# Kernel optimization log

Hardware: AMD Instinct MI355X
Metric: run time of the kernel (lower is better)

## Reference

```python
import jax, jax.numpy as jnp
import numpy as np

BS, SL, CL = 32, 512, 20      # batch, seq_len (visits), codes per visit
D, H, V = 256, 4, 20000       # d_model, heads, vocab_size
HD = D // H                   # size_per_head = 64
EPS = 1e-5


def make_pe_table(d_model, max_pos):
    # torch PositionalEncoding: sinusoidal table with a zero pad row prepended
    pe = np.array([[pos / np.power(10000, 2.0 * (j // 2) / d_model)
                    for j in range(d_model)] for pos in range(max_pos)])
    pe[:, 0::2] = np.sin(pe[:, 0::2])
    pe[:, 1::2] = np.cos(pe[:, 1::2])
    pe = np.concatenate([np.zeros((1, d_model)), pe], axis=0)
    return jnp.asarray(pe, dtype=jnp.float32)  # [max_pos+1, d]


def layer_norm(x, g, b):
    mu = jnp.mean(x, axis=-1, keepdims=True)
    var = jnp.mean(jnp.square(x - mu), axis=-1, keepdims=True)
    return (x - mu) * jax.lax.rsqrt(var + EPS) * g + b


def setup_inputs() -> dict:
    key = jax.random.key(0)
    ks = jax.random.split(key, 12)
    input_seqs = jax.random.randint(ks[0], (BS, SL, CL), 0, V, dtype=jnp.int32)
    masks = jnp.ones((BS, SL, SL), dtype=jnp.int32)
    lengths = jax.random.randint(ks[1], (BS,), 1, SL + 1, dtype=jnp.int32)
    seq_time_step = jax.random.uniform(ks[2], (BS, SL), dtype=jnp.float32)
    code_masks = jax.random.uniform(ks[3], (BS, SL, CL), dtype=jnp.float32)

    emb_table = jax.random.normal(ks[4], (V + 1, D), dtype=jnp.float32) * 0.02
    emb_table = emb_table.at[V].set(0.0)  # padding_idx row (never indexed here)
    bound = 1.0 / np.sqrt(V)
    bias_emb = jax.random.uniform(ks[5], (D,), minval=-bound, maxval=bound, dtype=jnp.float32)
    s = 1.0 / np.sqrt(D)
    Wq = jax.random.uniform(ks[6], (D, D), minval=-s, maxval=s, dtype=jnp.float32)
    Wk = jax.random.uniform(ks[7], (D, D), minval=-s, maxval=s, dtype=jnp.float32)
    Wv = jax.random.uniform(ks[8], (D, D), minval=-s, maxval=s, dtype=jnp.float32)
    Wfc = jax.random.uniform(ks[9], (D, D), minval=-s, maxval=s, dtype=jnp.float32)
    ln_g = jnp.ones((D,), dtype=jnp.float32)
    ln_b = jnp.zeros((D,), dtype=jnp.float32)
    so = 1.0 / np.sqrt(4 * D)
    out_w = jax.random.uniform(ks[10], (2, 4 * D), minval=-so, maxval=so, dtype=jnp.float32)
    out_b = jax.random.uniform(ks[11], (2,), minval=-so, maxval=so, dtype=jnp.float32)
    pe_table = make_pe_table(D, SL)

    return dict(input_seqs=input_seqs, masks=masks, lengths=lengths,
                seq_time_step=seq_time_step, code_masks=code_masks,
                emb_table=emb_table, bias_emb=bias_emb, pe_table=pe_table,
                Wq=Wq, Wk=Wk, Wv=Wv, Wfc=Wfc, ln_g=ln_g, ln_b=ln_b,
                out_w=out_w, out_b=out_b)


def reference(input_seqs, masks, lengths, seq_time_step, code_masks,
              emb_table, bias_emb, pe_table, Wq, Wk, Wv, Wfc,
              ln_g, ln_b, out_w, out_b):
    bs, sl, _ = input_seqs.shape
    # visit embedding: sum of code embeddings + bias  -> [bs, sl, d]
    x = emb_table[input_seqs].sum(axis=2) + bias_emb
    # positional encoding: pos ids = 1..len, 0 beyond length
    t_idx = jnp.arange(sl, dtype=jnp.int32)
    pos_ids = jnp.where(t_idx[None, :] < lengths[:, None], t_idx[None, :] + 1, 0)
    x = x + pe_table[pos_ids]
    res = x
    # manual MHA -- NOTE faithful to original: view(bs, H, sl, hd) directly
    q = (x @ Wq.T).reshape(bs, H, sl, HD)
    k = (x @ Wk.T).reshape(bs, H, sl, HD)
    v = (x @ Wv.T).reshape(bs, H, sl, HD)
    energy = jnp.einsum('bhqd,bhkd->bhqk', q, k) / np.sqrt(HD)
    energy = jnp.where(masks[:, None, :, :] == 0, -jnp.inf, energy)
    attn = jax.nn.softmax(energy, axis=-1)
    o = jnp.einsum('bhqk,bhkd->bhqd', attn, v)          # [bs,H,sl,hd]
    o = o.transpose(0, 2, 1, 3).reshape(bs, sl, D)
    x = layer_norm(o @ Wfc.T + res, ln_g, ln_b)
    # zero out positions >= length
    valid = (t_idx[None, :] < lengths[:, None])          # [bs, sl]
    x = jnp.where(valid[:, :, None], x, 0.0)
    # triangular-weighted temporal pooling into 4 bins (vectorized loops)
    lens = lengths.astype(jnp.float32)
    t = jnp.arange(1, sl + 1, dtype=jnp.float32)
    s_val = 4.0 * t[None, :] / lens[:, None]             # [bs, sl]
    m = jnp.arange(1, 5, dtype=jnp.float32)              # 4 bins
    w = jnp.square(1.0 - jnp.abs(s_val[:, :, None] - m[None, None, :]) / 4.0)  # [bs,sl,4]
    U = jnp.einsum('bsm,bsd->bmd', w, x)                 # [bs,4,d]
    U = U.reshape(bs, 4 * D)
    return U @ out_w.T + out_b                           # [bs, 2]
```

## Files before the change

kernel.cpp:

```cpp
#include <hip/hip_runtime.h>

#define BSZ 32
#define SLEN 512
#define CLEN 20
#define DMOD 256
#define NH 4
#define HDIM 64

typedef _Float16 half8 __attribute__((ext_vector_type(8)));
typedef _Float16 half4 __attribute__((ext_vector_type(4)));
typedef float float4v __attribute__((ext_vector_type(4)));

#define MFMA16(a, b, c) __builtin_amdgcn_mfma_f32_16x16x32_f16(a, b, c, 0, 0, 0)
#define PG(fi) ((((fi) >> 4) * 17) + ((fi) & 15))

__global__ __launch_bounds__(256) void k_cast(
    const float* __restrict__ W0, const float* __restrict__ W1,
    const float* __restrict__ W2, const float* __restrict__ W3,
    const float* __restrict__ emb,
    _Float16* __restrict__ wh, _Float16* __restrict__ embh) {
  const int bid = blockIdx.x;
  const float* src;
  _Float16* dst;
  int idx;
  if (bid < 128) {
    const int z = bid >> 5;
    src = (z == 0) ? W0 : (z == 1) ? W1 : (z == 2) ? W2 : W3;
    dst = wh + (size_t)z * 65536;
    idx = ((bid & 31) * 256 + threadIdx.x) * 8;
  } else {
    src = emb;
    dst = embh;
    idx = ((bid - 128) * 256 + threadIdx.x) * 8;
  }
  float v[8];
  *(float4*)v = *(const float4*)(src + idx);
  *(float4*)(v + 4) = *(const float4*)(src + idx + 4);
  half8 h;
  #pragma unroll
  for (int i = 0; i < 8; ++i) h[i] = (_Float16)v[i];
  *(half8*)(dst + idx) = h;
}

__global__ __launch_bounds__(256) void k_embed(
    const int* __restrict__ seqs, const int* __restrict__ lengths,
    const _Float16* __restrict__ embh, const float* __restrict__ bias,
    const float* __restrict__ pe, _Float16* __restrict__ x) {
  const int row0 = blockIdx.x * 8;
  const int sub = threadIdx.x >> 5;
  const int hl = threadIdx.x & 31;
  const int row = row0 + sub;
  const int b = row >> 9, s = row & 511;
  __shared__ int codes[8][CLEN];
  if (threadIdx.x < 8 * CLEN)
    codes[threadIdx.x / CLEN][threadIdx.x % CLEN] = seqs[row0 * CLEN + threadIdx.x];
  __syncthreads();
  const int pos = (s < lengths[b]) ? (s + 1) : 0;
  const int d = hl * 8;
  float acc[8];
  *(float4*)acc = *(const float4*)(bias + d);
  *(float4*)(acc + 4) = *(const float4*)(bias + d + 4);
  const float4 pv0 = *(const float4*)(pe + (size_t)pos * DMOD + d);
  const float4 pv1 = *(const float4*)(pe + (size_t)pos * DMOD + d + 4);
  acc[0] += pv0.x; acc[1] += pv0.y; acc[2] += pv0.z; acc[3] += pv0.w;
  acc[4] += pv1.x; acc[5] += pv1.y; acc[6] += pv1.z; acc[7] += pv1.w;
  #pragma unroll
  for (int c = 0; c < CLEN; ++c) {
    const half8 ev = *(const half8*)(embh + (size_t)codes[sub][c] * DMOD + d);
    #pragma unroll
    for (int i = 0; i < 8; ++i) acc[i] += (float)ev[i];
  }
  half8 hv;
  #pragma unroll
  for (int i = 0; i < 8; ++i) hv[i] = (_Float16)acc[i];
  *(half8*)(x + (size_t)row * DMOD + d) = hv;
}

__global__ __launch_bounds__(256) void k_maskpack(
    const int* __restrict__ masks, unsigned int* __restrict__ pk) {
  const int row0 = blockIdx.x * 8;
  const int wv = threadIdx.x >> 6;
  const int lane = threadIdx.x & 63;
  #pragma unroll
  for (int p = 0; p < 16; ++p) {
    const int it = wv + p * 4;
    const int r = row0 + (it >> 3);
    const int chunk = it & 7;
    const int m = masks[(size_t)r * SLEN + chunk * 64 + lane];
    const unsigned long long bal = __ballot(m != 0);
    if (lane == 0) {
      pk[(size_t)r * 16 + chunk * 2]     = (unsigned int)bal;
      pk[(size_t)r * 16 + chunk * 2 + 1] = (unsigned int)(bal >> 32);
    }
  }
}

__global__ __launch_bounds__(256) void k_gemm_qkv(
    const _Float16* __restrict__ A, const _Float16* __restrict__ Wb,
    _Float16* __restrict__ q, _Float16* __restrict__ k, _Float16* __restrict__ v) {
  const int z = blockIdx.z;
  _Float16* Cb = (z == 0) ? q : (z == 1) ? k : v;
  const _Float16* w_ = Wb + (size_t)z * 65536;
  const int m0 = blockIdx.x * 128;
  const int n0 = blockIdx.y * 128;
  const int tid = threadIdx.x;
  const int lane = tid & 63;
  const int w = tid >> 6;
  const int wm = (w >> 1) * 4;
  const int wn = (w & 1) * 4;
  __shared__ _Float16 smem[8704];
  half8* As = (half8*)(smem);
  half8* Ws = (half8*)(smem + 4096);
  float4v acc[4][4];
  #pragma unroll
  for (int i = 0; i < 4; ++i)
    #pragma unroll
    for (int j = 0; j < 4; ++j)
      acc[i][j] = (float4v){0.f, 0.f, 0.f, 0.f};
  int li_[2]; size_t ga_[2], gw_[2];
  #pragma unroll
  for (int p = 0; p < 2; ++p) {
    const int c = tid + p * 256;
    const int r = c & 127, qd = c >> 7;
    li_[p] = (r >> 4) * 64 + qd * 16 + (r & 15);
    ga_[p] = (size_t)(m0 + r) * DMOD + qd * 8;
    gw_[p] = (size_t)(n0 + r) * DMOD + qd * 8;
  }
  half8 pa[2], pw[2];
  #pragma unroll
  for (int p = 0; p < 2; ++p) {
    pa[p] = *(const half8*)(A + ga_[p]);
    pw[p] = *(const half8*)(w_ + gw_[p]);
  }
  for (int k0 = 0; k0 < DMOD; k0 += 32) {
    #pragma unroll
    for (int p = 0; p < 2; ++p) {
      As[li_[p]] = pa[p];
      Ws[li_[p]] = pw[p];
    }
    __syncthreads();
    if (k0 + 32 < DMOD) {
      #pragma unroll
      for (int p = 0; p < 2; ++p) {
        pa[p] = *(const half8*)(A + ga_[p] + k0 + 32);
        pw[p] = *(const half8*)(w_ + gw_[p] + k0 + 32);
      }
    }
    half8 af[4], wf[4];
    #pragma unroll
    for (int i = 0; i < 4; ++i) {
      af[i] = As[(wm + i) * 64 + lane];
      wf[i] = Ws[(wn + i) * 64 + lane];
    }
    #pragma unroll
    for (int i = 0; i < 4; ++i)
      #pragma unroll
      for (int j = 0; j < 4; ++j)
        acc[i][j] = MFMA16(af[i], wf[j], acc[i][j]);
    __syncthreads();
  }
  const int cr = (lane >> 4) * 4;
  const int cc = lane & 15;
  _Float16* Eh = smem;
  #pragma unroll
  for (int ip = 0; ip < 4; ++ip) {
    #pragma unroll
    for (int j = 0; j < 4; ++j) {
      const int col = (wn + j) * 16 + cc;
      #pragma unroll
      for (int r = 0; r < 4; ++r)
        Eh[((w >> 1) * 16 + cr + r) * 136 + col] = (_Float16)acc[ip][j][r];
    }
    __syncthreads();
    #pragma unroll
    for (int e = 0; e < 2; ++e) {
      const int idx = tid + e * 256;
      const int lr = idx >> 4;
      const int cg = idx & 15;
      const int gr = m0 + (lr >> 4) * 64 + ip * 16 + (lr & 15);
      *(half8*)(Cb + (size_t)gr * DMOD + n0 + cg * 8) =
          *(const half8*)&Eh[lr * 136 + cg * 8];
    }
    __syncthreads();
  }
}

__global__ __launch_bounds__(256) void k_vt(
    const _Float16* __restrict__ v, _Float16* __restrict__ vt) {
  const int bh = blockIdx.x;
  const size_t off = (size_t)bh * 32768;
  __shared__ _Float16 Th[64][66];
  const int tid = threadIdx.x;
  const int sc = blockIdx.y * 64;
  #pragma unroll
  for (int p = 0; p < 2; ++p) {
    const int lin = tid + p * 256;
    const int r = lin >> 3, g = lin & 7;
    *(half8*)&Th[r][g * 8] = *(const half8*)(v + off + (size_t)(sc + r) * 64 + g * 8);
  }
  __syncthreads();
  #pragma unroll
  for (int p = 0; p < 2; ++p) {
    const int lin = tid + p * 256;
    const int d = lin >> 3, sg = lin & 7;
    half8 hv;
    #pragma unroll
    for (int j = 0; j < 8; ++j) hv[j] = Th[sg * 8 + j][d];
    *(half8*)(vt + off + (size_t)d * 512 + sc + sg * 8) = hv;
  }
}

__global__ __launch_bounds__(256) void k_gemm_fc(
    const _Float16* __restrict__ A, const _Float16* __restrict__ w_,
    float* __restrict__ C, const _Float16* __restrict__ res) {
  const int m0 = blockIdx.x * 128;
  const int n0 = blockIdx.y * 128;
  const int tid = threadIdx.x;
  const int lane = tid & 63;
  const int w = tid >> 6;
  const int wm = (w >> 1) * 4;
  const int wn = (w & 1) * 4;
  __shared__ half8 As[512], Ws[512];
  float4v acc[4][4];
  #pragma unroll
  for (int i = 0; i < 4; ++i)
    #pragma unroll
    for (int j = 0; j < 4; ++j)
      acc[i][j] = (float4v){0.f, 0.f, 0.f, 0.f};
  int li_[2]; size_t ga_[2], gw_[2];
  #pragma unroll
  for (int p = 0; p < 2; ++p) {
    const int c = tid + p * 256;
    const int r = c & 127, qd = c >> 7;
    li_[p] = (r >> 4) * 64 + qd * 16 + (r & 15);
    ga_[p] = (size_t)(m0 + r) * DMOD + qd * 8;
    gw_[p] = (size_t)(n0 + r) * DMOD + qd * 8;
  }
  half8 pa[2], pw[2];
  #pragma unroll
  for (int p = 0; p < 2; ++p) {
    pa[p] = *(const half8*)(A + ga_[p]);
    pw[p] = *(const half8*)(w_ + gw_[p]);
  }
  for (int k0 = 0; k0 < DMOD; k0 += 32) {
    #pragma unroll
    for (int p = 0; p < 2; ++p) {
      As[li_[p]] = pa[p];
      Ws[li_[p]] = pw[p];
    }
    __syncthreads();
    if (k0 + 32 < DMOD) {
      #pragma unroll
      for (int p = 0; p < 2; ++p) {
        pa[p] = *(const half8*)(A + ga_[p] + k0 + 32);
        pw[p] = *(const half8*)(w_ + gw_[p] + k0 + 32);
      }
    }
    half8 af[4], wf[4];
    #pragma unroll
    for (int i = 0; i < 4; ++i) {
      af[i] = As[(wm + i) * 64 + lane];
      wf[i] = Ws[(wn + i) * 64 + lane];
    }
    #pragma unroll
    for (int i = 0; i < 4; ++i)
      #pragma unroll
      for (int j = 0; j < 4; ++j)
        acc[i][j] = MFMA16(af[i], wf[j], acc[i][j]);
    __syncthreads();
  }
  const int cr = (lane >> 4) * 4;
  const int cc = lane & 15;
  #pragma unroll
  for (int i = 0; i < 4; ++i) {
    const int gm = m0 + (wm + i) * 16 + cr;
    #pragma unroll
    for (int j = 0; j < 4; ++j) {
      const int gc = n0 + (wn + j) * 16 + cc;
      #pragma unroll
      for (int r = 0; r < 4; ++r) {
        const size_t flat = (size_t)(gm + r) * DMOD + gc;
        C[flat] = acc[i][j][r] + (float)res[flat];
      }
    }
  }
}

__global__ __launch_bounds__(256, 2) void k_attn(
    const _Float16* __restrict__ q_, const _Float16* __restrict__ k_,
    const _Float16* __restrict__ vt, const unsigned int* __restrict__ pk,
    _Float16* __restrict__ o) {
  const int L = blockIdx.x;
  const int bh = (L & 7) * 16 + ((L >> 3) & 15);
  const int q0 = (L >> 7) * 128;
  const size_t bhoff = (size_t)bh * 32768;
  __shared__ half8 QP[1088];
  __shared__ half8 Ks[544], Vs[544];
  __shared__ unsigned long long Ms64[128];
  __shared__ float Ps[4][128];
  __shared__ float lsum[128];
  const int tid = threadIdx.x;
  const int w = tid >> 6;
  const int lane = tid & 63;
  const int l15 = lane & 15;
  const int quad = lane >> 4;
  #pragma unroll
  for (int p = 0; p < 4; ++p) {
    const int lin = tid + p * 256;
    const int r = lin >> 3, g = lin & 7;
    const int fi = (r >> 4) * 128 + g * 16 + (r & 15);
    QP[PG(fi)] = *(const half8*)(q_ + bhoff + (size_t)(q0 + r) * 64 + g * 8);
  }
  __syncthreads();
  half8 qf[8][2];
  #pragma unroll
  for (int ns = 0; ns < 8; ++ns) {
    const int gq = ns * 8 + quad;
    qf[ns][0] = QP[gq * 17 + l15];
    qf[ns][1] = QP[(gq + 4) * 17 + l15];
  }
  float4v oacc[8];
  float lsw[8] = {0.f, 0.f, 0.f, 0.f, 0.f, 0.f, 0.f, 0.f};
  #pragma unroll
  for (int ns = 0; ns < 8; ++ns) oacc[ns] = (float4v){0.f, 0.f, 0.f, 0.f};
  for (int kc = 0; kc < SLEN; kc += 64) {
    __syncthreads();
    #pragma unroll
    for (int p = 0; p < 2; ++p) {
      const int lin = tid + p * 256;
      const int r = lin >> 3, g = lin & 7;
      const int fi = PG((r >> 4) * 128 + g * 16 + (r & 15));
      Ks[fi] = *(const half8*)(k_ + bhoff + (size_t)(kc + r) * 64 + g * 8);
      Vs[fi] = *(const half8*)(vt + bhoff + (size_t)r * 512 + kc + g * 8);
    }
    ((unsigned int*)Ms64)[tid] =
        pk[((size_t)((bh >> 2) << 9) + q0 + (tid >> 1)) * 16 + (kc >> 5) + (tid & 1)];
    __syncthreads();
    const int ga0 = (w * 8 + quad) * 17 + l15;
    const int ga1 = (w * 8 + quad + 4) * 17 + l15;
    const half8 ah0 = Ks[ga0], ah1 = Ks[ga1];
    #pragma unroll
    for (int ns = 0; ns < 8; ++ns) {
      float4v s = (float4v){0.f, 0.f, 0.f, 0.f};
      s = MFMA16(ah0, qf[ns][0], s);
      s = MFMA16(ah1, qf[ns][1], s);
      const int q = ns * 16 + l15;
      const unsigned long long mrow = Ms64[q];
      const unsigned mbits = (unsigned)(mrow >> (w * 16 + quad * 4)) & 15u;
      half4 h4;
      #pragma unroll
      for (int r = 0; r < 4; ++r) {
        const float pe = ((mbits >> r) & 1u) ? __expf(s[r] * 0.125f) : 0.f;
        h4[r] = (_Float16)pe;
        lsw[ns] += pe;
      }
      const int hb = ((ns * 8 + w * 2 + (quad >> 1)) * 17 + l15) * 8 + (quad & 1) * 4;
      *(half4*)((_Float16*)QP + hb) = h4;
    }
    __syncthreads();
    const half8 vh0 = Vs[ga0], vh1 = Vs[ga1];
    #pragma unroll
    for (int ns = 0; ns < 8; ++ns) {
      const int pb0 = (ns * 8 + quad) * 17 + l15;
      const int pb1 = (ns * 8 + quad + 4) * 17 + l15;
      oacc[ns] = MFMA16(vh0, QP[pb0], oacc[ns]);
      oacc[ns] = MFMA16(vh1, QP[pb1], oacc[ns]);
    }
  }
  #pragma unroll
  for (int ns = 0; ns < 8; ++ns) {
    lsw[ns] += __shfl_xor(lsw[ns], 16);
    lsw[ns] += __shfl_xor(lsw[ns], 32);
  }
  __syncthreads();
  if (quad == 0) {
    #pragma unroll
    for (int ns = 0; ns < 8; ++ns) Ps[w][ns * 16 + l15] = lsw[ns];
  }
  __syncthreads();
  if (tid < 128) lsum[tid] = Ps[0][tid] + Ps[1][tid] + Ps[2][tid] + Ps[3][tid];
  __syncthreads();
  const int b = bh >> 2, h = bh & 3;
  _Float16* Ot = (_Float16*)QP;
  #pragma unroll
  for (int ns = 0; ns < 8; ++ns) {
    const int q = ns * 16 + l15;
    const float inv = 1.0f / lsum[q];
    half4 h4;
    #pragma unroll
    for (int r = 0; r < 4; ++r) h4[r] = (_Float16)(oacc[ns][r] * inv);
    *(half4*)&Ot[q * 68 + w * 16 + quad * 4] = h4;
  }
  __syncthreads();
  #pragma unroll
  for (int e = 0; e < 4; ++e) {
    const int idx = tid + e * 256;
    const int qq = idx >> 3, g = idx & 7;
    *(half8*)(o + ((size_t)(b * SLEN + q0 + qq)) * DMOD + h * HDIM + g * 8) =
        *(const half8*)&Ot[qq * 68 + g * 8];
  }
}

__global__ __launch_bounds__(256) void k_lnpool(
    const float* __restrict__ Y, const int* __restrict__ lengths,
    const float* __restrict__ g, const float* __restrict__ bb,
    float* __restrict__ Up) {
  const int b = blockIdx.x;
  const int c = blockIdx.y;
  const int tid = threadIdx.x;
  const int w = tid >> 6;
  const int lane = tid & 63;
  __shared__ float Pl[4][4][DMOD];
  const int len = lengths[b];
  const float inv4 = 4.0f / (float)len;
  float gg[4], bv[4];
  *(float4*)gg = *(const float4*)(g + lane * 4);
  *(float4*)bv = *(const float4*)(bb + lane * 4);
  float a[4][4] = {};
  for (int t = 0; t < 8; ++t) {
    const int r = c * 32 + t * 4 + w;
    float v[4];
    *(float4*)v = *(const float4*)(Y + ((size_t)b * SLEN + r) * DMOD + lane * 4);
    float sum = v[0] + v[1] + v[2] + v[3];
    float sq = v[0] * v[0] + v[1] * v[1] + v[2] * v[2] + v[3] * v[3];
    #pragma unroll
    for (int off = 32; off > 0; off >>= 1) {
      sum += __shfl_xor(sum, off);
      sq += __shfl_xor(sq, off);
    }
    const float mu = sum * (1.0f / DMOD);
    const float inv = rsqrtf(sq * (1.0f / DMOD) - mu * mu + 1e-5f);
    const bool valid = r < len;
    float ov[4];
    #pragma unroll
    for (int i = 0; i < 4; ++i)
      ov[i] = valid ? ((v[i] - mu) * inv * gg[i] + bv[i]) : 0.f;
    const float sv = (float)(r + 1) * inv4;
    #pragma unroll
    for (int m = 0; m < 4; ++m) {
      const float tm = 1.0f - fabsf(sv - (float)(m + 1)) * 0.25f;
      const float t2 = tm * tm;
      #pragma unroll
      for (int i = 0; i < 4; ++i) a[m][i] += t2 * ov[i];
    }
  }
  #pragma unroll
  for (int m = 0; m < 4; ++m)
    *(float4*)&Pl[w][m][lane * 4] = *(float4*)a[m];
  __syncthreads();
  #pragma unroll
  for (int e = 0; e < 4; ++e) {
    const int idx = tid + e * 256;
    const int m = idx >> 8, d = idx & 255;
    const float s = Pl[0][m][d] + Pl[1][m][d] + Pl[2][m][d] + Pl[3][m][d];
    Up[(((size_t)b * 16 + c) * 4 + m) * DMOD + d] = s;
  }
}

__global__ __launch_bounds__(256) void k_out(
    const float* __restrict__ Up, const float* __restrict__ ow,
    const float* __restrict__ ob, float* __restrict__ out) {
  const int b = blockIdx.x;
  const int tid = threadIdx.x;
  const int w = tid >> 6;
  const int lane = tid & 63;
  __shared__ float rr[8];
  float4 s = {0.f, 0.f, 0.f, 0.f};
  #pragma unroll
  for (int c = 0; c < 16; ++c) {
    const float4 u = *(const float4*)(Up + ((size_t)b * 16 + c) * 1024 + tid * 4);
    s.x += u.x; s.y += u.y; s.z += u.z; s.w += u.w;
  }
  const float4 w0 = *(const float4*)(ow + tid * 4);
  const float4 w1 = *(const float4*)(ow + 1024 + tid * 4);
  float acc0 = s.x * w0.x + s.y * w0.y + s.z * w0.z + s.w * w0.w;
  float acc1 = s.x * w1.x + s.y * w1.y + s.z * w1.z + s.w * w1.w;
  #pragma unroll
  for (int off = 32; off > 0; off >>= 1) {
    acc0 += __shfl_xor(acc0, off);
    acc1 += __shfl_xor(acc1, off);
  }
  if (lane == 0) { rr[w] = acc0; rr[4 + w] = acc1; }
  __syncthreads();
  if (tid == 0) {
    out[b * 2 + 0] = rr[0] + rr[1] + rr[2] + rr[3] + ob[0];
    out[b * 2 + 1] = rr[4] + rr[5] + rr[6] + rr[7] + ob[1];
  }
}

extern "C" void kernel_launch(void* const* d_in, const int* in_sizes, int n_in,
                              void* d_out, int out_size, void* d_ws, size_t ws_size,
                              hipStream_t stream) {
  const int* seqs     = (const int*)d_in[0];
  const int* masks    = (const int*)d_in[1];
  const int* lengths  = (const int*)d_in[2];
  const float* emb    = (const float*)d_in[5];
  const float* bias   = (const float*)d_in[6];
  const float* pe     = (const float*)d_in[7];
  const float* Wq     = (const float*)d_in[8];
  const float* Wk     = (const float*)d_in[9];
  const float* Wv     = (const float*)d_in[10];
  const float* Wfc    = (const float*)d_in[11];
  const float* ln_g   = (const float*)d_in[12];
  const float* ln_b   = (const float*)d_in[13];
  const float* out_w  = (const float*)d_in[14];
  const float* out_b  = (const float*)d_in[15];
  float* outp = (float*)d_out;

  const size_t NE = (size_t)BSZ * SLEN * DMOD;
  _Float16* q = (_Float16*)d_ws;
  _Float16* k = q + NE;
  _Float16* v = k + NE;
  _Float16* vt = v + NE;
  _Float16* x = vt + NE;
  _Float16* o = x + NE;
  _Float16* wh = o + NE;
  unsigned int* pk = (unsigned int*)(wh + 4 * 65536);
  float* Up = (float*)(pk + BSZ * SLEN * 16);
  float* y = (float*)q;
  _Float16* embh = (_Float16*)d_ws;

  k_cast<<<2628, 256, 0, stream>>>(Wq, Wk, Wv, Wfc, emb, wh, embh);
  k_embed<<<BSZ * SLEN / 8, 256, 0, stream>>>(seqs, lengths, embh, bias, pe, x);
  k_maskpack<<<BSZ * SLEN / 8, 256, 0, stream>>>(masks, pk);
  k_gemm_qkv<<<dim3(128, 2, 3), 256, 0, stream>>>(x, wh, q, k, v);
  k_vt<<<dim3(BSZ * NH, 8), 256, 0, stream>>>(v, vt);
  k_attn<<<BSZ * NH * (SLEN / 128), 256, 0, stream>>>(q, k, vt, pk, o);
  k_gemm_fc<<<dim3(128, 2), 256, 0, stream>>>(o, wh + 3 * 65536, y, x);
  k_lnpool<<<dim3(BSZ, 16), 256, 0, stream>>>(y, lengths, ln_g, ln_b, Up);
  k_out<<<BSZ, 256, 0, stream>>>(Up, out_w, out_b, outp);
}
```

Before: 220.0 us.

## Fuse mask packing into embed kernel and widen attention blocks to 256 queries

The mask bit-packing kernel is merged into the embedding kernel, removing one launch. The attention kernel now uses 512-thread blocks, each covering 256 queries as two 128-query halves. Both halves share one K/V tile staged in shared memory, which halves K/V global loads and per-chunk staging. In exchange the grid shrinks to 256 blocks at one block per CU, which lowers occupancy and adds barrier cost across 8 waves.

```diff
diff --git a/kernel.cpp b/kernel.cpp
--- a/kernel.cpp
+++ b/kernel.cpp
@@ -42,10 +42,11 @@
   *(half8*)(dst + idx) = h;
 }
 
-__global__ __launch_bounds__(256) void k_embed(
+__global__ __launch_bounds__(256) void k_embmask(
     const int* __restrict__ seqs, const int* __restrict__ lengths,
     const _Float16* __restrict__ embh, const float* __restrict__ bias,
-    const float* __restrict__ pe, _Float16* __restrict__ x) {
+    const float* __restrict__ pe, _Float16* __restrict__ x,
+    const int* __restrict__ masks, unsigned int* __restrict__ pk) {
   const int row0 = blockIdx.x * 8;
   const int sub = threadIdx.x >> 5;
   const int hl = threadIdx.x & 31;
@@ -74,11 +75,6 @@
   #pragma unroll
   for (int i = 0; i < 8; ++i) hv[i] = (_Float16)acc[i];
   *(half8*)(x + (size_t)row * DMOD + d) = hv;
-}
-
-__global__ __launch_bounds__(256) void k_maskpack(
-    const int* __restrict__ masks, unsigned int* __restrict__ pk) {
-  const int row0 = blockIdx.x * 8;
   const int wv = threadIdx.x >> 6;
   const int lane = threadIdx.x & 63;
   #pragma unroll
@@ -286,49 +282,52 @@
   }
 }
 
-__global__ __launch_bounds__(256, 2) void k_attn(
+__global__ __launch_bounds__(512, 1) void k_attn(
     const _Float16* __restrict__ q_, const _Float16* __restrict__ k_,
     const _Float16* __restrict__ vt, const unsigned int* __restrict__ pk,
     _Float16* __restrict__ o) {
   const int L = blockIdx.x;
-  const int bh = (L & 7) * 16 + ((L >> 3) & 15);
-  const int q0 = (L >> 7) * 128;
+  const int bh = L >> 1;
+  const int q0 = (L & 1) * 256;
   const size_t bhoff = (size_t)bh * 32768;
-  __shared__ half8 QP[1088];
+  __shared__ half8 QP[2][1088];
   __shared__ half8 Ks[544], Vs[544];
-  __shared__ unsigned long long Ms64[128];
-  __shared__ float Ps[4][128];
-  __shared__ float lsum[128];
+  __shared__ unsigned long long Ms64[256];
+  __shared__ float Ps[2][4][128];
+  __shared__ float lsum[256];
   const int tid = threadIdx.x;
-  const int w = tid >> 6;
+  const int w8 = tid >> 6;
+  const int qh = w8 >> 2;
+  const int w = w8 & 3;
   const int lane = tid & 63;
   const int l15 = lane & 15;
   const int quad = lane >> 4;
   #pragma unroll
   for (int p = 0; p < 4; ++p) {
-    const int lin = tid + p * 256;
+    const int lin = tid + p * 512;
     const int r = lin >> 3, g = lin & 7;
-    const int fi = (r >> 4) * 128 + g * 16 + (r & 15);
-    QP[PG(fi)] = *(const half8*)(q_ + bhoff + (size_t)(q0 + r) * 64 + g * 8);
+    const int rh = r >> 7, rl = r & 127;
+    const int fi = (rl >> 4) * 128 + g * 16 + (rl & 15);
+    QP[rh][PG(fi)] = *(const half8*)(q_ + bhoff + (size_t)(q0 + r) * 64 + g * 8);
   }
   __syncthreads();
   half8 qf[8][2];
   #pragma unroll
   for (int ns = 0; ns < 8; ++ns) {
     const int gq = ns * 8 + quad;
-    qf[ns][0] = QP[gq * 17 + l15];
-    qf[ns][1] = QP[(gq + 4) * 17 + l15];
+    qf[ns][0] = QP[qh][gq * 17 + l15];
+    qf[ns][1] = QP[qh][(gq + 4) * 17 + l15];
   }
   float4v oacc[8];
   float lsw[8] = {0.f, 0.f, 0.f, 0.f, 0.f, 0.f, 0.f, 0.f};
   #pragma unroll
   for (int ns = 0; ns < 8; ++ns) oacc[ns] = (float4v){0.f, 0.f, 0.f, 0.f};
+  const int ga0 = (w * 8 + quad) * 17 + l15;
+  const int ga1 = (w * 8 + quad + 4) * 17 + l15;
   for (int kc = 0; kc < SLEN; kc += 64) {
     __syncthreads();
-    #pragma unroll
-    for (int p = 0; p < 2; ++p) {
-      const int lin = tid + p * 256;
-      const int r = lin >> 3, g = lin & 7;
+    {
+      const int r = tid >> 3, g = tid & 7;
       const int fi = PG((r >> 4) * 128 + g * 16 + (r & 15));
       Ks[fi] = *(const half8*)(k_ + bhoff + (size_t)(kc + r) * 64 + g * 8);
       Vs[fi] = *(const half8*)(vt + bhoff + (size_t)r * 512 + kc + g * 8);
@@ -336,8 +335,6 @@
     ((unsigned int*)Ms64)[tid] =
         pk[((size_t)((bh >> 2) << 9) + q0 + (tid >> 1)) * 16 + (kc >> 5) + (tid & 1)];
     __syncthreads();
-    const int ga0 = (w * 8 + quad) * 17 + l15;
-    const int ga1 = (w * 8 + quad + 4) * 17 + l15;
     const half8 ah0 = Ks[ga0], ah1 = Ks[ga1];
     #pragma unroll
     for (int ns = 0; ns < 8; ++ns) {
@@ -345,7 +342,7 @@
       s = MFMA16(ah0, qf[ns][0], s);
       s = MFMA16(ah1, qf[ns][1], s);
       const int q = ns * 16 + l15;
-      const unsigned long long mrow = Ms64[q];
+      const unsigned long long mrow = Ms64[qh * 128 + q];
       const unsigned mbits = (unsigned)(mrow >> (w * 16 + quad * 4)) & 15u;
       half4 h4;
       #pragma unroll
@@ -355,7 +352,7 @@
         lsw[ns] += pe;
       }
       const int hb = ((ns * 8 + w * 2 + (quad >> 1)) * 17 + l15) * 8 + (quad & 1) * 4;
-      *(half4*)((_Float16*)QP + hb) = h4;
+      *(half4*)((_Float16*)QP[qh] + hb) = h4;
     }
     __syncthreads();
     const half8 vh0 = Vs[ga0], vh1 = Vs[ga1];
@@ -363,8 +360,8 @@
     for (int ns = 0; ns < 8; ++ns) {
       const int pb0 = (ns * 8 + quad) * 17 + l15;
       const int pb1 = (ns * 8 + quad + 4) * 17 + l15;
-      oacc[ns] = MFMA16(vh0, QP[pb0], oacc[ns]);
-      oacc[ns] = MFMA16(vh1, QP[pb1], oacc[ns]);
+      oacc[ns] = MFMA16(vh0, QP[qh][pb0], oacc[ns]);
+      oacc[ns] = MFMA16(vh1, QP[qh][pb1], oacc[ns]);
     }
   }
   #pragma unroll
@@ -375,16 +372,19 @@
   __syncthreads();
   if (quad == 0) {
     #pragma unroll
-    for (int ns = 0; ns < 8; ++ns) Ps[w][ns * 16 + l15] = lsw[ns];
-  }
-  __syncthreads();
-  if (tid < 128) lsum[tid] = Ps[0][tid] + Ps[1][tid] + Ps[2][tid] + Ps[3][tid];
+    for (int ns = 0; ns < 8; ++ns) Ps[qh][w][ns * 16 + l15] = lsw[ns];
+  }
+  __syncthreads();
+  if (tid < 256) {
+    const int hh = tid >> 7, qq = tid & 127;
+    lsum[tid] = Ps[hh][0][qq] + Ps[hh][1][qq] + Ps[hh][2][qq] + Ps[hh][3][qq];
+  }
   __syncthreads();
   const int b = bh >> 2, h = bh & 3;
   _Float16* Ot = (_Float16*)QP;
   #pragma unroll
   for (int ns = 0; ns < 8; ++ns) {
-    const int q = ns * 16 + l15;
+    const int q = qh * 128 + ns * 16 + l15;
     const float inv = 1.0f / lsum[q];
     half4 h4;
     #pragma unroll
@@ -394,7 +394,7 @@
   __syncthreads();
   #pragma unroll
   for (int e = 0; e < 4; ++e) {
-    const int idx = tid + e * 256;
+    const int idx = tid + e * 512;
     const int qq = idx >> 3, g = idx & 7;
     *(half8*)(o + ((size_t)(b * SLEN + q0 + qq)) * DMOD + h * HDIM + g * 8) =
         *(const half8*)&Ot[qq * 68 + g * 8];
@@ -521,11 +521,11 @@
   _Float16* embh = (_Float16*)d_ws;
 
   k_cast<<<2628, 256, 0, stream>>>(Wq, Wk, Wv, Wfc, emb, wh, embh);
-  k_embed<<<BSZ * SLEN / 8, 256, 0, stream>>>(seqs, lengths, embh, bias, pe, x);
-  k_maskpack<<<BSZ * SLEN / 8, 256, 0, stream>>>(masks, pk);
+  k_embmask<<<BSZ * SLEN / 8, 256, 0, stream>>>(seqs, lengths, embh, bias, pe, x,
+                                                masks, pk);
   k_gemm_qkv<<<dim3(128, 2, 3), 256, 0, stream>>>(x, wh, q, k, v);
   k_vt<<<dim3(BSZ * NH, 8), 256, 0, stream>>>(v, vt);
-  k_attn<<<BSZ * NH * (SLEN / 128), 256, 0, stream>>>(q, k, vt, pk, o);
+  k_attn<<<BSZ * NH * (SLEN / 256), 512, 0, stream>>>(q, k, vt, pk, o);
   k_gemm_fc<<<dim3(128, 2), 256, 0, stream>>>(o, wh + 3 * 65536, y, x);
   k_lnpool<<<dim3(BSZ, 16), 256, 0, stream>>>(y, lengths, ln_g, ln_b, Up);
   k_out<<<BSZ, 256, 0, stream>>>(Up, out_w, out_b, outp);
```

After: 223.6 us. About the same (+1.7%).
